# Kernel tuning notes

Hardware: AMD Instinct MI355X
Metric: run time of the kernel (lower is better)

Reference implementation:

```python
import jax, jax.numpy as jnp
import numpy as np

HEAD = 8
SR = 4
LN_EPS = 1e-5


def setup_inputs() -> dict:
    key = jax.random.key(0)
    ks = jax.random.split(key, 8)
    B, H, W, d = 4, 64, 64, 512
    s = 0.02
    inp = {
        "x": jax.random.normal(ks[0], (B, 1, H * W, d), jnp.float32),
        "Wq": jax.random.normal(ks[1], (d, d), jnp.float32) * s,
        "bq": jnp.zeros((d,), jnp.float32),
        "Wk": jax.random.normal(ks[2], (d, d), jnp.float32) * s,
        "bk": jnp.zeros((d,), jnp.float32),
        "Wv": jax.random.normal(ks[3], (d, d), jnp.float32) * s,
        "bv": jnp.zeros((d,), jnp.float32),
        "Wp": jax.random.normal(ks[4], (d, d), jnp.float32) * s,
        "bp": jnp.zeros((d,), jnp.float32),
        # spatial-reduction conv kernel, HWIO layout: [SR, SR, d, d]
        "Wsr": jax.random.normal(ks[5], (SR, SR, d, d), jnp.float32) * s,
        "bsr": jnp.zeros((d,), jnp.float32),
        "gamma": jnp.ones((d,), jnp.float32),
        "beta": jnp.zeros((d,), jnp.float32),
        "H": H,
        "W": W,
    }
    return inp


def _heads(t, B, N, dh):
    # [B, N, C] -> [B, HEAD, N, dh] ; channels split as (head, dh)
    return t.reshape(B, N, HEAD, dh).transpose(0, 2, 1, 3)


def reference(x, Wq, bq, Wk, bk, Wv, bv, Wp, bp, Wsr, bsr, gamma, beta, H, W):
    B = x.shape[0]
    C = x.shape[-1]
    dh = C // HEAD
    scale = dh ** (-0.5)
    N = H * W

    x_img = x.reshape(B, H, W, C)  # channels-last (equiv. to torch b c h w)

    # q projection (Q.Linear over channel dim)
    q = _heads((x_img @ Wq.T + bq).reshape(B, N, C), B, N, dh)  # [B,head,N,dh]

    # spatial reduction: strided conv (kernel=stride=SR) + LayerNorm over channels
    x_sr = jax.lax.conv_general_dilated(
        x_img, Wsr, window_strides=(SR, SR), padding="VALID",
        dimension_numbers=("NHWC", "HWIO", "NHWC")) + bsr  # [B,H/SR,W/SR,C]
    mu = x_sr.mean(axis=-1, keepdims=True)
    var = ((x_sr - mu) ** 2).mean(axis=-1, keepdims=True)
    x_kv = (x_sr - mu) * jax.lax.rsqrt(var + LN_EPS) * gamma + beta

    Nk = x_kv.shape[1] * x_kv.shape[2]
    x_kv = x_kv.reshape(B, Nk, C)
    k = _heads(x_kv @ Wk.T + bk, B, Nk, dh)  # [B,head,Nk,dh]
    v = _heads(x_kv @ Wv.T + bv, B, Nk, dh)  # [B,head,Nk,dh]

    attn = jnp.einsum("bhqd,bhkd->bhqk", q, k) * scale
    attn = jax.nn.softmax(attn, axis=-1)
    out = jnp.einsum("bhqk,bhkd->bhqd", attn, v)  # [B,head,N,dh]

    out = out.transpose(0, 2, 1, 3).reshape(B, N, C)
    out = out @ Wp.T + bp
    return out.reshape(B, 1, N, C)
```

## Files before the change

### kernel.cpp

```cpp
#include <hip/hip_runtime.h>


typedef __bf16 bf16x8 __attribute__((ext_vector_type(8)));
typedef float f32x4 __attribute__((ext_vector_type(4)));

__device__ __forceinline__ ushort f2bf(float v) {
  uint u = __float_as_uint(v);
  return (ushort)((u + 0x7FFFu + ((u >> 16) & 1u)) >> 16);
}
__device__ __forceinline__ float bf2f(ushort h) {
  return __uint_as_float((uint)h << 16);
}
__device__ __forceinline__ void gload16(const void* g, void* l) {
  __builtin_amdgcn_global_load_lds(
      (const __attribute__((address_space(1))) void*)g,
      (__attribute__((address_space(3))) void*)l, 16, 0, 0);
}
__device__ __forceinline__ int xcd_swz(int bid, int nwg) {
  int cpx = nwg >> 3;
  return (bid & 7) * cpx + (bid >> 3);
}

__global__ __launch_bounds__(256) void prep_kernel(
    const float* __restrict__ x, const float* __restrict__ Wq,
    const float* __restrict__ Wp, const float* __restrict__ Wk,
    const float* __restrict__ Wv, const float* __restrict__ Wsr,
    const float* __restrict__ bk, const float* __restrict__ bv,
    ushort* __restrict__ xq, ushort* __restrict__ Wq_,
    ushort* __restrict__ Wp_, ushort* __restrict__ Wkv_,
    ushort* __restrict__ Wsr_, float* __restrict__ bkv) {
  __shared__ float t[32][33];
  int bid = blockIdx.x, tid = threadIdx.x;
  if (bid < 4096 + 512) {
    const float* src;
    ushort* dst;
    int gid;
    bool full = false;
    if (bid < 4096) {
      src = x; dst = xq; gid = bid * 256 + tid;
    } else {
      int z = (bid - 4096) >> 7;
      src = (z == 0) ? Wq : (z == 1) ? Wp : (z == 2) ? Wk : Wv;
      dst = (z == 0) ? Wq_ : (z == 1) ? Wp_ : (z == 2) ? Wkv_ : (Wkv_ + 512 * 1024);
      gid = ((bid - 4096) & 127) * 256 + tid;
      full = (z >= 2);
    }
    int row = gid >> 6, c8 = (gid & 63) << 3;
    float4 a = *(const float4*)(src + (size_t)row * 512 + c8);
    float4 b = *(const float4*)(src + (size_t)row * 512 + c8 + 4);
    ushort h[8], l[8];
    float vv[8] = {a.x, a.y, a.z, a.w, b.x, b.y, b.z, b.w};
#pragma unroll
    for (int e = 0; e < 8; ++e) { h[e] = f2bf(vv[e]); l[e] = f2bf(vv[e] - bf2f(h[e])); }
    uint4 hp, lp;
    hp.x = h[0] | ((uint)h[1] << 16); hp.y = h[2] | ((uint)h[3] << 16);
    hp.z = h[4] | ((uint)h[5] << 16); hp.w = h[6] | ((uint)h[7] << 16);
    lp.x = l[0] | ((uint)l[1] << 16); lp.y = l[2] | ((uint)l[3] << 16);
    lp.z = l[4] | ((uint)l[5] << 16); lp.w = l[6] | ((uint)l[7] << 16);
    if (full) {
      *(uint4*)(dst + (size_t)row * 1024 + c8) = hp;
      *(uint4*)(dst + (size_t)row * 1024 + 512 + c8) = lp;
    } else {
      *(uint4*)(dst + (size_t)row * 512 + c8) = hp;
    }
  } else if (bid < 4096 + 512 + 4096) {
    int tb = bid - 4608;
    int z = tb >> 8, rem = tb & 255;
    int ci0 = (rem >> 4) << 5, co0 = (rem & 15) << 5;
    int tx = tid & 31, ty = tid >> 5;
#pragma unroll
    for (int i = 0; i < 32; i += 8)
      t[ty + i][tx] = Wsr[((size_t)z * 512 + ci0 + ty + i) * 512 + co0 + tx];
    __syncthreads();
#pragma unroll
    for (int i = 0; i < 32; i += 8) {
      float v = t[tx][ty + i];
      int co = co0 + ty + i, ci = ci0 + tx;
      Wsr_[((size_t)z * 512 + co) * 512 + ci] = f2bf(v);
    }
  } else {
    bkv[tid] = bk[tid]; bkv[tid + 256] = bk[tid + 256];
    bkv[tid + 512] = bv[tid]; bkv[tid + 768] = bv[tid + 256];
  }
}

template <int EPI, int TERMS>
__device__ __forceinline__ void gemm_body(
    const ushort* __restrict__ A, const ushort* __restrict__ Bw,
    const float* __restrict__ bias, float* __restrict__ C,
    ushort* __restrict__ Qs, ushort* __restrict__ Kq, ushort* __restrict__ Vt,
    int N, int bx, int by, ushort* lds) {
  constexpr int NS = (TERMS == 1) ? 8 : TERMS * 8;
  constexpr int AST = (TERMS == 1) ? 512 : 1024;
  int tid = threadIdx.x;
  int lane = tid & 63, w = tid >> 6;
  int wr = w >> 1, wc = w & 1;
  int l15 = lane & 15, g = lane >> 4;
  int srow = lane >> 3;
  int scol = (lane & 7) ^ srow;

  const ushort* aBase = A + (size_t)(by * 128 + w * 32 + srow) * AST + scol * 8;
  const ushort* bBase = Bw + (size_t)(bx * 128 + w * 32 + srow) * AST + scol * 8;

  f32x4 acc[4][4];
#pragma unroll
  for (int i = 0; i < 4; ++i)
#pragma unroll
    for (int j = 0; j < 4; ++j) acc[i][j] = (f32x4){0.f, 0.f, 0.f, 0.f};

#define STAGE_G(ks, buf)                                              \
  {                                                                   \
    int kk = (ks) * 64;                                               \
    int ap = (TERMS == 1) ? kk : kk - (kk >= 1024 ? 1024 : 0);        \
    int bp = (TERMS == 1) ? kk : kk - (kk >= 512 ? 512 : 0);          \
    ushort* aD = lds + (buf) * 16384 + w * 2048;                      \
    ushort* bD = lds + (buf) * 16384 + 8192 + w * 2048;               \
    _Pragma("unroll") for (int t = 0; t < 4; ++t) {                   \
      gload16(aBase + (size_t)t * 8 * AST + ap, aD + t * 512);        \
      gload16(bBase + (size_t)t * 8 * AST + bp, bD + t * 512);        \
    }                                                                 \
  }

#define COMPUTE_G(buf)                                                         \
  {                                                                            \
    const ushort* As = lds + (buf) * 16384;                                    \
    const ushort* Bs = As + 8192;                                              \
    _Pragma("unroll") for (int kk2 = 0; kk2 < 2; ++kk2) {                      \
      int rb = kk2 * 4 + g;                                                    \
      bf16x8 af[4], bg[4];                                                     \
      _Pragma("unroll") for (int i = 0; i < 4; ++i) {                          \
        int row = wr * 64 + i * 16 + l15;                                      \
        af[i] = *(const bf16x8*)&As[row * 64 + ((rb ^ (row & 7)) << 3)];       \
      }                                                                        \
      _Pragma("unroll") for (int j = 0; j < 4; ++j) {                          \
        int col = wc * 64 + j * 16 + l15;                                      \
        bg[j] = *(const bf16x8*)&Bs[col * 64 + ((rb ^ (col & 7)) << 3)];       \
      }                                                                        \
      _Pragma("unroll") for (int i = 0; i < 4; ++i)                            \
        _Pragma("unroll") for (int j = 0; j < 4; ++j)                          \
          acc[i][j] =                                                          \
              __builtin_amdgcn_mfma_f32_16x16x32_bf16(af[i], bg[j], acc[i][j], \
                                                      0, 0, 0);                \
    }                                                                          \
  }

  STAGE_G(0, 0);
  __syncthreads();
  for (int ks = 0; ks < NS - 1; ++ks) {
    STAGE_G(ks + 1, (ks + 1) & 1);
    COMPUTE_G(ks & 1);
    __syncthreads();
  }
  COMPUTE_G((NS - 1) & 1);

#undef STAGE_G
#undef COMPUTE_G

  if (EPI == 0) {
#pragma unroll
    for (int j = 0; j < 4; ++j) {
      int col = bx * 128 + wc * 64 + j * 16 + l15;
      float bj = bias ? bias[col] : 0.f;
#pragma unroll
      for (int i = 0; i < 4; ++i) {
        int row0 = by * 128 + wr * 64 + i * 16 + g * 4;
#pragma unroll
        for (int r = 0; r < 4; ++r)
          C[(size_t)(row0 + r) * N + col] = acc[i][j][r] + bj;
      }
    }
  } else if (EPI == 1) {
    __syncthreads();
#pragma unroll
    for (int j = 0; j < 4; ++j) {
      int cl = wc * 64 + j * 16 + l15;
      float bj = bias[bx * 128 + cl];
#pragma unroll
      for (int i = 0; i < 4; ++i) {
        int rl0 = wr * 64 + i * 16 + g * 4;
#pragma unroll
        for (int r = 0; r < 4; ++r) {
          float v = (acc[i][j][r] + bj) * 0.125f;
          ushort h = f2bf(v), lo = f2bf(v - bf2f(h));
          lds[(rl0 + r) * 128 + cl] = h;
          lds[16384 + (rl0 + r) * 128 + cl] = lo;
        }
      }
    }
    __syncthreads();
#pragma unroll
    for (int it = 0; it < 8; ++it) {
      int c = tid + it * 256;
      int r = c >> 4, ck = c & 15;
      int grow = by * 128 + r;
      size_t base = ((size_t)grow * 8 + bx * 2 + (ck >> 3)) * 128 + (ck & 7) * 8;
      *(uint4*)(Qs + base) = *(const uint4*)&lds[r * 128 + ck * 8];
      *(uint4*)(Qs + base + 64) = *(const uint4*)&lds[16384 + r * 128 + ck * 8];
    }
  } else {
#pragma unroll
    for (int j = 0; j < 4; ++j) {
      int col = bx * 128 + wc * 64 + j * 16 + l15;
      float bj = bias[col];
      bool isK = col < 512;
      int cp = isK ? col : col - 512;
      int hh = cp >> 6, d = cp & 63;
#pragma unroll
      for (int i = 0; i < 4; ++i) {
        int row0 = by * 128 + wr * 64 + i * 16 + g * 4;
#pragma unroll
        for (int r = 0; r < 4; ++r) {
          int row = row0 + r;
          int b = row >> 8, kk = row & 255;
          float v = acc[i][j][r] + bj;
          ushort h = f2bf(v), lo = f2bf(v - bf2f(h));
          if (isK) {
            size_t base = ((size_t)((b * 8 + hh) * 256) + kk) * 128 + d;
            Kq[base] = h; Kq[base + 64] = lo;
          } else {
            size_t base = ((size_t)((b * 8 + hh) * 64) + d) * 512 + kk;
            Vt[base] = h; Vt[base + 256] = lo;
          }
        }
      }
    }
  }
}

__device__ __forceinline__ void conv_body(
    const ushort* __restrict__ xq, const ushort* __restrict__ Wsr_,
    float* __restrict__ part, int bx, int by, int z, ushort* lds) {
  int kh = z >> 2, kw = z & 3;
  int tid = threadIdx.x;
  int lane = tid & 63, w = tid >> 6;
  int wr = w >> 1, wc = w & 1;
  int l15 = lane & 15, g = lane >> 4;
  int srow = lane >> 3;
  int scol = (lane & 7) ^ srow;

  const ushort* aBase[4];
#pragma unroll
  for (int t = 0; t < 4; ++t) {
    int gm = by * 128 + w * 32 + t * 8 + srow;
    int xr = (gm >> 8) * 4096 + ((((gm >> 4) & 15) << 2) + kh) * 64 +
             ((gm & 15) << 2) + kw;
    aBase[t] = xq + (size_t)xr * 512 + scol * 8;
  }
  const ushort* bBase =
      Wsr_ + ((size_t)(z * 512 + bx * 128 + w * 32 + srow)) * 512 + scol * 8;

  f32x4 acc[4][4];
#pragma unroll
  for (int i = 0; i < 4; ++i)
#pragma unroll
    for (int j = 0; j < 4; ++j) acc[i][j] = (f32x4){0.f, 0.f, 0.f, 0.f};

#define STAGE_C(ks, buf)                                              \
  {                                                                   \
    int kk = (ks) * 64;                                               \
    ushort* aD = lds + (buf) * 16384 + w * 2048;                      \
    ushort* bD = lds + (buf) * 16384 + 8192 + w * 2048;               \
    _Pragma("unroll") for (int t = 0; t < 4; ++t) {                   \
      gload16(aBase[t] + kk, aD + t * 512);                           \
      gload16(bBase + (size_t)t * 4096 + kk, bD + t * 512);           \
    }                                                                 \
  }

#define COMPUTE_C(buf)                                                         \
  {                                                                            \
    const ushort* As = lds + (buf) * 16384;                                    \
    const ushort* Bs = As + 8192;                                              \
    _Pragma("unroll") for (int kk2 = 0; kk2 < 2; ++kk2) {                      \
      int rb = kk2 * 4 + g;                                                    \
      bf16x8 af[4], bg[4];                                                     \
      _Pragma("unroll") for (int i = 0; i < 4; ++i) {                          \
        int row = wr * 64 + i * 16 + l15;                                      \
        af[i] = *(const bf16x8*)&As[row * 64 + ((rb ^ (row & 7)) << 3)];       \
      }                                                                        \
      _Pragma("unroll") for (int j = 0; j < 4; ++j) {                          \
        int col = wc * 64 + j * 16 + l15;                                      \
        bg[j] = *(const bf16x8*)&Bs[col * 64 + ((rb ^ (col & 7)) << 3)];       \
      }                                                                        \
      _Pragma("unroll") for (int i = 0; i < 4; ++i)                            \
        _Pragma("unroll") for (int j = 0; j < 4; ++j)                          \
          acc[i][j] =                                                          \
              __builtin_amdgcn_mfma_f32_16x16x32_bf16(af[i], bg[j], acc[i][j], \
                                                      0, 0, 0);                \
    }                                                                          \
  }

  STAGE_C(0, 0);
  __syncthreads();
  for (int ks = 0; ks < 7; ++ks) {
    STAGE_C(ks + 1, (ks + 1) & 1);
    COMPUTE_C(ks & 1);
    __syncthreads();
  }
  COMPUTE_C(1);

#undef STAGE_C
#undef COMPUTE_C

  float* Cp = part + (size_t)z * 524288;
#pragma unroll
  for (int j = 0; j < 4; ++j) {
    int col = bx * 128 + wc * 64 + j * 16 + l15;
#pragma unroll
    for (int i = 0; i < 4; ++i) {
      int row0 = by * 128 + wr * 64 + i * 16 + g * 4;
#pragma unroll
      for (int r = 0; r < 4; ++r)
        Cp[(size_t)(row0 + r) * 512 + col] = acc[i][j][r];
    }
  }
}

__global__ __launch_bounds__(256) void conv_kernel(
    const ushort* __restrict__ xq, const ushort* __restrict__ Wsr_,
    float* __restrict__ part) {
  __shared__ __align__(16) ushort lds[32768];
  int bid = xcd_swz(blockIdx.x, 512);
  conv_body(xq, Wsr_, part, bid & 3, (bid >> 2) & 7, bid >> 5, lds);
}

__global__ __launch_bounds__(256) void qkv_kernel(
    const ushort* __restrict__ xq, const ushort* __restrict__ Wq_,
    const float* __restrict__ bq, ushort* __restrict__ Qs,
    const ushort* __restrict__ xkv_, const ushort* __restrict__ Wkv_,
    const float* __restrict__ bkv, ushort* __restrict__ Kq,
    ushort* __restrict__ Vt) {
  __shared__ __align__(16) ushort lds[32768];
  int n = blockIdx.x;
  int xcd = n & 7, slot = n >> 3;
  if (slot < 8) {
    int id = xcd * 8 + slot;
    gemm_body<2, 3>(xkv_, Wkv_, bkv, nullptr, nullptr, Kq, Vt, 1024,
                    id & 7, id >> 3, lds);
  } else {
    int id = xcd * 64 + (slot - 8);
    gemm_body<1, 1>(xq, Wq_, bq, nullptr, Qs, nullptr, nullptr, 512,
                    id & 3, id >> 2, lds);
  }
}

__global__ __launch_bounds__(256) void gemm_out_kernel(
    const ushort* __restrict__ A, const ushort* __restrict__ Bw,
    const float* __restrict__ bias, float* __restrict__ C) {
  __shared__ __align__(16) ushort lds[32768];
  int bid = xcd_swz(blockIdx.x, 512);
  gemm_body<0, 1>(A, Bw, bias, C, nullptr, nullptr, nullptr, 512,
                  bid & 3, bid >> 2, lds);
}

__global__ __launch_bounds__(256) void ln_kernel(
    const float* __restrict__ part, const float* __restrict__ bsr,
    const float* __restrict__ gamma, const float* __restrict__ beta,
    ushort* __restrict__ xkv_) {
  int row = blockIdx.x;
  int t = threadIdx.x;
  float v0 = bsr[t], v1 = bsr[t + 256];
  for (int p = 0; p < 16; ++p) {
    v0 += part[(size_t)p * 524288 + (size_t)row * 512 + t];
    v1 += part[(size_t)p * 524288 + (size_t)row * 512 + t + 256];
  }
  float s = v0 + v1, sq = v0 * v0 + v1 * v1;
#pragma unroll
  for (int o = 1; o < 64; o <<= 1) {
    s += __shfl_xor(s, o);
    sq += __shfl_xor(sq, o);
  }
  __shared__ float red[8];
  int wv = t >> 6;
  if ((t & 63) == 0) { red[wv] = s; red[4 + wv] = sq; }
  __syncthreads();
  s = red[0] + red[1] + red[2] + red[3];
  sq = red[4] + red[5] + red[6] + red[7];
  float mu = s * (1.0f / 512.0f);
  float var = sq * (1.0f / 512.0f) - mu * mu;
  float rs = rsqrtf(var + 1e-5f);
  float y0 = (v0 - mu) * rs * gamma[t] + beta[t];
  float y1 = (v1 - mu) * rs * gamma[t + 256] + beta[t + 256];
  ushort h0 = f2bf(y0), h1 = f2bf(y1);
  xkv_[(size_t)row * 1024 + t] = h0;
  xkv_[(size_t)row * 1024 + t + 256] = h1;
  xkv_[(size_t)row * 1024 + 512 + t] = f2bf(y0 - bf2f(h0));
  xkv_[(size_t)row * 1024 + 512 + t + 256] = f2bf(y1 - bf2f(h1));
}

__global__ __launch_bounds__(256, 2) void attn_kernel(
    const ushort* __restrict__ Qs, const ushort* __restrict__ Kq,
    const ushort* __restrict__ Vt, ushort* __restrict__ attno) {
  __shared__ __align__(16) char arena[65536];
  ushort* KsL = (ushort*)arena;
  ushort* VtL = (ushort*)(arena + 16384);
  ushort* PL = (ushort*)(arena + 49152);
  float* ob = (float*)arena;

  int tid = threadIdx.x;
  int qb = blockIdx.x, h = blockIdx.y, b = blockIdx.z;
  int n0 = qb * 128, bh = b * 8 + h;
  int lane = tid & 63, w = tid >> 6;
  int q15 = lane & 15, g = lane >> 4;

  const ushort* kbase = Kq + (size_t)bh * 256 * 128;
  const ushort* vbase = Vt + (size_t)bh * 64 * 512;

  bf16x8 qf[2][2][2];
#pragma unroll
  for (int set = 0; set < 2; ++set) {
    const ushort* qptr =
        Qs + ((size_t)(b * 4096 + n0 + set * 64 + w * 16 + q15) * 8 + h) * 128;
#pragma unroll
    for (int s = 0; s < 2; ++s)
#pragma unroll
      for (int kb = 0; kb < 2; ++kb)
        qf[set][s][kb] = *(const bf16x8*)(qptr + s * 64 + kb * 32 + g * 8);
  }

  f32x4 accO[2][4];
#pragma unroll
  for (int set = 0; set < 2; ++set)
#pragma unroll
    for (int t = 0; t < 4; ++t) accO[set][t] = (f32x4){0.f, 0.f, 0.f, 0.f};
  float m[2] = {-1e30f, -1e30f}, l[2] = {0.f, 0.f};

#define STAGE_A(cc, buf)                                                     \
  {                                                                          \
    _Pragma("unroll") for (int i = 0; i < 2; ++i) {                          \
      int rb_ = w * 16 + i * 8;                                              \
      int r_ = rb_ + (lane >> 3);                                            \
      int sb_ = (lane & 7) ^ (r_ & 7);                                       \
      gload16(kbase + (size_t)((cc) * 64 + r_) * 128 + (sb_ << 3),           \
              KsL + (buf) * 4096 + rb_ * 64);                                \
    }                                                                        \
    _Pragma("unroll") for (int i = 0; i < 4; ++i) {                          \
      int rb_ = w * 16 + i * 4;                                              \
      int r_ = rb_ + (lane >> 4);                                            \
      int sb_ = (lane & 15) ^ (r_ & 7);                                      \
      gload16(vbase + (size_t)r_ * 512 + ((sb_ >> 3) << 8) + (cc) * 64 +     \
                  ((sb_ & 7) << 3),                                          \
              VtL + (buf) * 8192 + rb_ * 128);                               \
    }                                                                        \
  }

  STAGE_A(0, 0);
  __syncthreads();

  for (int c = 0; c < 4; ++c) {
    int buf = c & 1;
    if (c < 3) STAGE_A(c + 1, buf ^ 1);
    const ushort* Ks = KsL + buf * 4096;
    const ushort* Vs = VtL + buf * 8192;

    f32x4 accS[2][4];
#pragma unroll
    for (int set = 0; set < 2; ++set)
#pragma unroll
      for (int t = 0; t < 4; ++t) accS[set][t] = (f32x4){0.f, 0.f, 0.f, 0.f};
#pragma unroll
    for (int kb = 0; kb < 2; ++kb) {
      bf16x8 ak[4];
#pragma unroll
      for (int t = 0; t < 4; ++t) {
        int kkr = t * 16 + q15;
        ak[t] = *(const bf16x8*)&Ks[kkr * 64 + (((kb * 4 + g) ^ (kkr & 7)) << 3)];
      }
#pragma unroll
      for (int set = 0; set < 2; ++set) {
#pragma unroll
        for (int t = 0; t < 4; ++t)
          accS[set][t] = __builtin_amdgcn_mfma_f32_16x16x32_bf16(
              ak[t], qf[set][0][kb], accS[set][t], 0, 0, 0);
#pragma unroll
        for (int t = 0; t < 4; ++t)
          accS[set][t] = __builtin_amdgcn_mfma_f32_16x16x32_bf16(
              ak[t], qf[set][1][kb], accS[set][t], 0, 0, 0);
      }
    }

#pragma unroll
    for (int set = 0; set < 2; ++set) {
      int qrowL = set * 64 + w * 16 + q15;
      float mx = -1e30f;
#pragma unroll
      for (int t = 0; t < 4; ++t)
#pragma unroll
        for (int r = 0; r < 4; ++r) mx = fmaxf(mx, accS[set][t][r]);
      mx = fmaxf(mx, __shfl_xor(mx, 16));
      mx = fmaxf(mx, __shfl_xor(mx, 32));
      float mn = fmaxf(m[set], mx);
      float fac = __expf(m[set] - mn);
      m[set] = mn;
      float sum = 0.f;
      ushort ph[4][4];
#pragma unroll
      for (int t = 0; t < 4; ++t)
#pragma unroll
        for (int r = 0; r < 4; ++r) {
          float p = __expf(accS[set][t][r] - mn);
          ushort hp = f2bf(p);
          ph[t][r] = hp;
          sum += bf2f(hp);
        }
      sum += __shfl_xor(sum, 16);
      sum += __shfl_xor(sum, 32);
      l[set] = l[set] * fac + sum;
#pragma unroll
      for (int t = 0; t < 4; ++t) {
        accO[set][t][0] *= fac; accO[set][t][1] *= fac;
        accO[set][t][2] *= fac; accO[set][t][3] *= fac;
      }
#pragma unroll
      for (int t = 0; t < 4; ++t)
#pragma unroll
        for (int rp = 0; rp < 4; rp += 2) {
          uint u = ph[t][rp] | ((uint)ph[t][rp + 1] << 16);
          int kkl = t * 16 + g * 4 + rp;
          int blk = kkl >> 3, off = kkl & 7;
          *(uint*)((char*)PL + qrowL * 128 + ((blk ^ (q15 & 7)) << 4) + off * 2) = u;
        }
    }
    __syncthreads();

    bf16x8 pf[2][2];
#pragma unroll
    for (int set = 0; set < 2; ++set) {
      int qrowL = set * 64 + w * 16 + q15;
#pragma unroll
      for (int kb = 0; kb < 2; ++kb)
        pf[set][kb] = *(const bf16x8*)((char*)PL + qrowL * 128 +
                                       (((kb * 4 + g) ^ (q15 & 7)) << 4));
    }
#pragma unroll
    for (int s = 0; s < 2; ++s)
#pragma unroll
      for (int kb = 0; kb < 2; ++kb)
#pragma unroll
        for (int t = 0; t < 4; ++t) {
          int d = t * 16 + q15;
          bf16x8 vf =
              *(const bf16x8*)&Vs[d * 128 + (((s * 8 + kb * 4 + g) ^ (d & 7)) << 3)];
          accO[0][t] = __builtin_amdgcn_mfma_f32_16x16x32_bf16(vf, pf[0][kb],
                                                               accO[0][t], 0, 0, 0);
          accO[1][t] = __builtin_amdgcn_mfma_f32_16x16x32_bf16(vf, pf[1][kb],
                                                               accO[1][t], 0, 0, 0);
        }
    __syncthreads();
  }
#undef STAGE_A

#pragma unroll
  for (int set = 0; set < 2; ++set) {
    if (set) __syncthreads();
    float inv = 1.0f / l[set];
#pragma unroll
    for (int t = 0; t < 4; ++t)
#pragma unroll
      for (int r = 0; r < 4; ++r)
        ob[(t * 16 + g * 4 + r) * 68 + w * 16 + q15] = accO[set][t][r] * inv;
    __syncthreads();
#pragma unroll
    for (int i = 0; i < 2; ++i) {
      int idx = tid + i * 256;
      int qq = idx >> 3, d8 = (idx & 7) << 3;
      ushort hh[8];
#pragma unroll
      for (int jj = 0; jj < 8; ++jj) hh[jj] = f2bf(ob[(d8 + jj) * 68 + qq]);
      uint4 hp;
      hp.x = hh[0] | ((uint)hh[1] << 16); hp.y = hh[2] | ((uint)hh[3] << 16);
      hp.z = hh[4] | ((uint)hh[5] << 16); hp.w = hh[6] | ((uint)hh[7] << 16);
      size_t rowb = (size_t)(b * 4096 + n0 + set * 64 + qq) * 512 + h * 64 + d8;
      *(uint4*)(attno + rowb) = hp;
    }
  }
}

extern "C" void kernel_launch(void* const* d_in, const int* in_sizes, int n_in,
                              void* d_out, int out_size, void* d_ws, size_t ws_size,
                              hipStream_t stream) {
  const float* x     = (const float*)d_in[0];
  const float* Wq    = (const float*)d_in[1];
  const float* bq    = (const float*)d_in[2];
  const float* Wk    = (const float*)d_in[3];
  const float* bk    = (const float*)d_in[4];
  const float* Wv    = (const float*)d_in[5];
  const float* bv    = (const float*)d_in[6];
  const float* Wp    = (const float*)d_in[7];
  const float* bp    = (const float*)d_in[8];
  const float* Wsr   = (const float*)d_in[9];
  const float* bsr   = (const float*)d_in[10];
  const float* gamma = (const float*)d_in[11];
  const float* beta  = (const float*)d_in[12];

  float* ws = (float*)d_ws;
  ushort* xq     = (ushort*)ws;
  ushort* attno_ = (ushort*)ws;
  float*  conv_part = ws + 4194304;
  ushort* Qsplit = (ushort*)(ws + 4194304);
  ushort* Wsr_ = (ushort*)(ws + 12582912);
  float*  rest = ws + 14680064;
  ushort* Wq_  = (ushort*)rest;
  ushort* Wp_  = (ushort*)(rest + 131072);
  ushort* Wkv_ = (ushort*)(rest + 262144);
  ushort* xkv_ = (ushort*)(rest + 786432);
  ushort* Kq   = (ushort*)(rest + 1310720);
  ushort* Vt   = (ushort*)(rest + 1835008);
  float*  bkv  = rest + 2359296;
  float* outp = (float*)d_out;

  prep_kernel<<<8705, 256, 0, stream>>>(x, Wq, Wp, Wk, Wv, Wsr, bk, bv,
                                        xq, Wq_, Wp_, Wkv_, Wsr_, bkv);
  conv_kernel<<<512, 256, 0, stream>>>(xq, Wsr_, conv_part);
  ln_kernel<<<1024, 256, 0, stream>>>(conv_part, bsr, gamma, beta, xkv_);
  qkv_kernel<<<576, 256, 0, stream>>>(xq, Wq_, bq, Qsplit,
                                      xkv_, Wkv_, bkv, Kq, Vt);
  attn_kernel<<<dim3(32, 8, 4), 256, 0, stream>>>(Qsplit, Kq, Vt, attno_);
  gemm_out_kernel<<<512, 256, 0, stream>>>(attno_, Wp_, bp, outp);
}
```

Before: 120.1 us.

## Drop split-bf16 hi/lo compensation from K/V/Q paths, use plain bf16

Removes the two-term bf16 (hi+lo) representation previously used for Wk/Wv, xkv, Q, K and V, so every GEMM and the attention QK^T and PV products use single bf16 operands. This halves the K-dimension work in the KV projection and in the attention matmuls, shrinks the intermediate buffers and the attention LDS arena, and reduces global traffic. In exchange it loses the extra precision the compensation provided, which may affect accuracy against the fp32 reference.

```diff
diff --git a/kernel.cpp b/kernel.cpp
--- a/kernel.cpp
+++ b/kernel.cpp
@@ -35,34 +35,25 @@
     const float* src;
     ushort* dst;
     int gid;
-    bool full = false;
     if (bid < 4096) {
       src = x; dst = xq; gid = bid * 256 + tid;
     } else {
       int z = (bid - 4096) >> 7;
       src = (z == 0) ? Wq : (z == 1) ? Wp : (z == 2) ? Wk : Wv;
-      dst = (z == 0) ? Wq_ : (z == 1) ? Wp_ : (z == 2) ? Wkv_ : (Wkv_ + 512 * 1024);
+      dst = (z == 0) ? Wq_ : (z == 1) ? Wp_ : (z == 2) ? Wkv_ : (Wkv_ + 512 * 512);
       gid = ((bid - 4096) & 127) * 256 + tid;
-      full = (z >= 2);
     }
     int row = gid >> 6, c8 = (gid & 63) << 3;
     float4 a = *(const float4*)(src + (size_t)row * 512 + c8);
     float4 b = *(const float4*)(src + (size_t)row * 512 + c8 + 4);
-    ushort h[8], l[8];
+    ushort h[8];
     float vv[8] = {a.x, a.y, a.z, a.w, b.x, b.y, b.z, b.w};
 #pragma unroll
-    for (int e = 0; e < 8; ++e) { h[e] = f2bf(vv[e]); l[e] = f2bf(vv[e] - bf2f(h[e])); }
-    uint4 hp, lp;
+    for (int e = 0; e < 8; ++e) h[e] = f2bf(vv[e]);
+    uint4 hp;
     hp.x = h[0] | ((uint)h[1] << 16); hp.y = h[2] | ((uint)h[3] << 16);
     hp.z = h[4] | ((uint)h[5] << 16); hp.w = h[6] | ((uint)h[7] << 16);
-    lp.x = l[0] | ((uint)l[1] << 16); lp.y = l[2] | ((uint)l[3] << 16);
-    lp.z = l[4] | ((uint)l[5] << 16); lp.w = l[6] | ((uint)l[7] << 16);
-    if (full) {
-      *(uint4*)(dst + (size_t)row * 1024 + c8) = hp;
-      *(uint4*)(dst + (size_t)row * 1024 + 512 + c8) = lp;
-    } else {
-      *(uint4*)(dst + (size_t)row * 512 + c8) = hp;
-    }
+    *(uint4*)(dst + (size_t)row * 512 + c8) = hp;
   } else if (bid < 4096 + 512 + 4096) {
     int tb = bid - 4608;
     int z = tb >> 8, rem = tb & 255;
@@ -84,14 +75,12 @@
   }
 }
 
-template <int EPI, int TERMS>
+template <int EPI>
 __device__ __forceinline__ void gemm_body(
     const ushort* __restrict__ A, const ushort* __restrict__ Bw,
     const float* __restrict__ bias, float* __restrict__ C,
     ushort* __restrict__ Qs, ushort* __restrict__ Kq, ushort* __restrict__ Vt,
     int N, int bx, int by, ushort* lds) {
-  constexpr int NS = (TERMS == 1) ? 8 : TERMS * 8;
-  constexpr int AST = (TERMS == 1) ? 512 : 1024;
   int tid = threadIdx.x;
   int lane = tid & 63, w = tid >> 6;
   int wr = w >> 1, wc = w & 1;
@@ -99,8 +88,8 @@
   int srow = lane >> 3;
   int scol = (lane & 7) ^ srow;
 
-  const ushort* aBase = A + (size_t)(by * 128 + w * 32 + srow) * AST + scol * 8;
-  const ushort* bBase = Bw + (size_t)(bx * 128 + w * 32 + srow) * AST + scol * 8;
+  const ushort* aBase = A + (size_t)(by * 128 + w * 32 + srow) * 512 + scol * 8;
+  const ushort* bBase = Bw + (size_t)(bx * 128 + w * 32 + srow) * 512 + scol * 8;
 
   f32x4 acc[4][4];
 #pragma unroll
@@ -111,13 +100,11 @@
 #define STAGE_G(ks, buf)                                              \
   {                                                                   \
     int kk = (ks) * 64;                                               \
-    int ap = (TERMS == 1) ? kk : kk - (kk >= 1024 ? 1024 : 0);        \
-    int bp = (TERMS == 1) ? kk : kk - (kk >= 512 ? 512 : 0);          \
     ushort* aD = lds + (buf) * 16384 + w * 2048;                      \
     ushort* bD = lds + (buf) * 16384 + 8192 + w * 2048;               \
     _Pragma("unroll") for (int t = 0; t < 4; ++t) {                   \
-      gload16(aBase + (size_t)t * 8 * AST + ap, aD + t * 512);        \
-      gload16(bBase + (size_t)t * 8 * AST + bp, bD + t * 512);        \
+      gload16(aBase + (size_t)t * 4096 + kk, aD + t * 512);           \
+      gload16(bBase + (size_t)t * 4096 + kk, bD + t * 512);           \
     }                                                                 \
   }
 
@@ -146,12 +133,12 @@
 
   STAGE_G(0, 0);
   __syncthreads();
-  for (int ks = 0; ks < NS - 1; ++ks) {
+  for (int ks = 0; ks < 7; ++ks) {
     STAGE_G(ks + 1, (ks + 1) & 1);
     COMPUTE_G(ks & 1);
     __syncthreads();
   }
-  COMPUTE_G((NS - 1) & 1);
+  COMPUTE_G(1);
 
 #undef STAGE_G
 #undef COMPUTE_G
@@ -179,12 +166,8 @@
       for (int i = 0; i < 4; ++i) {
         int rl0 = wr * 64 + i * 16 + g * 4;
 #pragma unroll
-        for (int r = 0; r < 4; ++r) {
-          float v = (acc[i][j][r] + bj) * 0.125f;
-          ushort h = f2bf(v), lo = f2bf(v - bf2f(h));
-          lds[(rl0 + r) * 128 + cl] = h;
-          lds[16384 + (rl0 + r) * 128 + cl] = lo;
-        }
+        for (int r = 0; r < 4; ++r)
+          lds[(rl0 + r) * 128 + cl] = f2bf((acc[i][j][r] + bj) * 0.125f);
       }
     }
     __syncthreads();
@@ -193,9 +176,8 @@
       int c = tid + it * 256;
       int r = c >> 4, ck = c & 15;
       int grow = by * 128 + r;
-      size_t base = ((size_t)grow * 8 + bx * 2 + (ck >> 3)) * 128 + (ck & 7) * 8;
+      size_t base = ((size_t)grow * 8 + bx * 2 + (ck >> 3)) * 64 + (ck & 7) * 8;
       *(uint4*)(Qs + base) = *(const uint4*)&lds[r * 128 + ck * 8];
-      *(uint4*)(Qs + base + 64) = *(const uint4*)&lds[16384 + r * 128 + ck * 8];
     }
   } else {
 #pragma unroll
@@ -212,15 +194,11 @@
         for (int r = 0; r < 4; ++r) {
           int row = row0 + r;
           int b = row >> 8, kk = row & 255;
-          float v = acc[i][j][r] + bj;
-          ushort h = f2bf(v), lo = f2bf(v - bf2f(h));
-          if (isK) {
-            size_t base = ((size_t)((b * 8 + hh) * 256) + kk) * 128 + d;
-            Kq[base] = h; Kq[base + 64] = lo;
-          } else {
-            size_t base = ((size_t)((b * 8 + hh) * 64) + d) * 512 + kk;
-            Vt[base] = h; Vt[base + 256] = lo;
-          }
+          ushort h = f2bf(acc[i][j][r] + bj);
+          if (isK)
+            Kq[((size_t)((b * 8 + hh) * 256) + kk) * 64 + d] = h;
+          else
+            Vt[((size_t)((b * 8 + hh) * 64) + d) * 256 + kk] = h;
         }
       }
     }
@@ -334,12 +312,12 @@
   int xcd = n & 7, slot = n >> 3;
   if (slot < 8) {
     int id = xcd * 8 + slot;
-    gemm_body<2, 3>(xkv_, Wkv_, bkv, nullptr, nullptr, Kq, Vt, 1024,
-                    id & 7, id >> 3, lds);
+    gemm_body<2>(xkv_, Wkv_, bkv, nullptr, nullptr, Kq, Vt, 1024,
+                 id & 7, id >> 3, lds);
   } else {
     int id = xcd * 64 + (slot - 8);
-    gemm_body<1, 1>(xq, Wq_, bq, nullptr, Qs, nullptr, nullptr, 512,
-                    id & 3, id >> 2, lds);
+    gemm_body<1>(xq, Wq_, bq, nullptr, Qs, nullptr, nullptr, 512,
+                 id & 3, id >> 2, lds);
   }
 }
 
@@ -348,8 +326,8 @@
     const float* __restrict__ bias, float* __restrict__ C) {
   __shared__ __align__(16) ushort lds[32768];
   int bid = xcd_swz(blockIdx.x, 512);
-  gemm_body<0, 1>(A, Bw, bias, C, nullptr, nullptr, nullptr, 512,
-                  bid & 3, bid >> 2, lds);
+  gemm_body<0>(A, Bw, bias, C, nullptr, nullptr, nullptr, 512,
+               bid & 3, bid >> 2, lds);
 }
 
 __global__ __launch_bounds__(256) void ln_kernel(
@@ -378,22 +356,18 @@
   float mu = s * (1.0f / 512.0f);
   float var = sq * (1.0f / 512.0f) - mu * mu;
   float rs = rsqrtf(var + 1e-5f);
-  float y0 = (v0 - mu) * rs * gamma[t] + beta[t];
-  float y1 = (v1 - mu) * rs * gamma[t + 256] + beta[t + 256];
-  ushort h0 = f2bf(y0), h1 = f2bf(y1);
-  xkv_[(size_t)row * 1024 + t] = h0;
-  xkv_[(size_t)row * 1024 + t + 256] = h1;
-  xkv_[(size_t)row * 1024 + 512 + t] = f2bf(y0 - bf2f(h0));
-  xkv_[(size_t)row * 1024 + 512 + t + 256] = f2bf(y1 - bf2f(h1));
+  xkv_[(size_t)row * 512 + t] = f2bf((v0 - mu) * rs * gamma[t] + beta[t]);
+  xkv_[(size_t)row * 512 + t + 256] =
+      f2bf((v1 - mu) * rs * gamma[t + 256] + beta[t + 256]);
 }
 
 __global__ __launch_bounds__(256, 2) void attn_kernel(
     const ushort* __restrict__ Qs, const ushort* __restrict__ Kq,
     const ushort* __restrict__ Vt, ushort* __restrict__ attno) {
-  __shared__ __align__(16) char arena[65536];
+  __shared__ __align__(16) char arena[49152];
   ushort* KsL = (ushort*)arena;
   ushort* VtL = (ushort*)(arena + 16384);
-  ushort* PL = (ushort*)(arena + 49152);
+  ushort* PL = (ushort*)(arena + 32768);
   float* ob = (float*)arena;
 
   int tid = threadIdx.x;
@@ -402,19 +376,17 @@
   int lane = tid & 63, w = tid >> 6;
   int q15 = lane & 15, g = lane >> 4;
 
-  const ushort* kbase = Kq + (size_t)bh * 256 * 128;
-  const ushort* vbase = Vt + (size_t)bh * 64 * 512;
-
-  bf16x8 qf[2][2][2];
+  const ushort* kbase = Kq + (size_t)bh * 256 * 64;
+  const ushort* vbase = Vt + (size_t)bh * 64 * 256;
+
+  bf16x8 qf[2][2];
 #pragma unroll
   for (int set = 0; set < 2; ++set) {
     const ushort* qptr =
-        Qs + ((size_t)(b * 4096 + n0 + set * 64 + w * 16 + q15) * 8 + h) * 128;
-#pragma unroll
-    for (int s = 0; s < 2; ++s)
-#pragma unroll
-      for (int kb = 0; kb < 2; ++kb)
-        qf[set][s][kb] = *(const bf16x8*)(qptr + s * 64 + kb * 32 + g * 8);
+        Qs + ((size_t)(b * 4096 + n0 + set * 64 + w * 16 + q15) * 8 + h) * 64;
+#pragma unroll
+    for (int kb = 0; kb < 2; ++kb)
+      qf[set][kb] = *(const bf16x8*)(qptr + kb * 32 + g * 8);
   }
 
   f32x4 accO[2][4];
@@ -430,16 +402,10 @@
       int rb_ = w * 16 + i * 8;                                              \
       int r_ = rb_ + (lane >> 3);                                            \
       int sb_ = (lane & 7) ^ (r_ & 7);                                       \
-      gload16(kbase + (size_t)((cc) * 64 + r_) * 128 + (sb_ << 3),           \
+      gload16(kbase + (size_t)((cc) * 64 + r_) * 64 + (sb_ << 3),            \
               KsL + (buf) * 4096 + rb_ * 64);                                \
-    }                                                                        \
-    _Pragma("unroll") for (int i = 0; i < 4; ++i) {                          \
-      int rb_ = w * 16 + i * 4;                                              \
-      int r_ = rb_ + (lane >> 4);                                            \
-      int sb_ = (lane & 15) ^ (r_ & 7);                                      \
-      gload16(vbase + (size_t)r_ * 512 + ((sb_ >> 3) << 8) + (cc) * 64 +     \
-                  ((sb_ & 7) << 3),                                          \
-              VtL + (buf) * 8192 + rb_ * 128);                               \
+      gload16(vbase + (size_t)r_ * 256 + (cc) * 64 + (sb_ << 3),             \
+              VtL + (buf) * 4096 + rb_ * 64);                                \
     }                                                                        \
   }
 
@@ -450,7 +416,7 @@
     int buf = c & 1;
     if (c < 3) STAGE_A(c + 1, buf ^ 1);
     const ushort* Ks = KsL + buf * 4096;
-    const ushort* Vs = VtL + buf * 8192;
+    const ushort* Vs = VtL + buf * 4096;
 
     f32x4 accS[2][4];
 #pragma unroll
@@ -466,16 +432,11 @@
         ak[t] = *(const bf16x8*)&Ks[kkr * 64 + (((kb * 4 + g) ^ (kkr & 7)) << 3)];
       }
 #pragma unroll
-      for (int set = 0; set < 2; ++set) {
+      for (int set = 0; set < 2; ++set)
 #pragma unroll
         for (int t = 0; t < 4; ++t)
           accS[set][t] = __builtin_amdgcn_mfma_f32_16x16x32_bf16(
-              ak[t], qf[set][0][kb], accS[set][t], 0, 0, 0);
-#pragma unroll
-        for (int t = 0; t < 4; ++t)
-          accS[set][t] = __builtin_amdgcn_mfma_f32_16x16x32_bf16(
-              ak[t], qf[set][1][kb], accS[set][t], 0, 0, 0);
-      }
+              ak[t], qf[set][kb], accS[set][t], 0, 0, 0);
     }
 
 #pragma unroll
@@ -532,19 +493,17 @@
                                        (((kb * 4 + g) ^ (q15 & 7)) << 4));
     }
 #pragma unroll
-    for (int s = 0; s < 2; ++s)
-#pragma unroll
-      for (int kb = 0; kb < 2; ++kb)
-#pragma unroll
-        for (int t = 0; t < 4; ++t) {
-          int d = t * 16 + q15;
-          bf16x8 vf =
-              *(const bf16x8*)&Vs[d * 128 + (((s * 8 + kb * 4 + g) ^ (d & 7)) << 3)];
-          accO[0][t] = __builtin_amdgcn_mfma_f32_16x16x32_bf16(vf, pf[0][kb],
-                                                               accO[0][t], 0, 0, 0);
-          accO[1][t] = __builtin_amdgcn_mfma_f32_16x16x32_bf16(vf, pf[1][kb],
-                                                               accO[1][t], 0, 0, 0);
-        }
+    for (int kb = 0; kb < 2; ++kb)
+#pragma unroll
+      for (int t = 0; t < 4; ++t) {
+        int d = t * 16 + q15;
+        bf16x8 vf =
+            *(const bf16x8*)&Vs[d * 64 + (((kb * 4 + g) ^ (d & 7)) << 3)];
+        accO[0][t] = __builtin_amdgcn_mfma_f32_16x16x32_bf16(vf, pf[0][kb],
+                                                             accO[0][t], 0, 0, 0);
+        accO[1][t] = __builtin_amdgcn_mfma_f32_16x16x32_bf16(vf, pf[1][kb],
+                                                             accO[1][t], 0, 0, 0);
+      }
     __syncthreads();
   }
 #undef STAGE_A
@@ -602,10 +561,10 @@
   ushort* Wq_  = (ushort*)rest;
   ushort* Wp_  = (ushort*)(rest + 131072);
   ushort* Wkv_ = (ushort*)(rest + 262144);
-  ushort* xkv_ = (ushort*)(rest + 786432);
-  ushort* Kq   = (ushort*)(rest + 1310720);
-  ushort* Vt   = (ushort*)(rest + 1835008);
-  float*  bkv  = rest + 2359296;
+  ushort* xkv_ = (ushort*)(rest + 524288);
+  ushort* Kq   = (ushort*)(rest + 786432);
+  ushort* Vt   = (ushort*)(rest + 1048576);
+  float*  bkv  = rest + 1310720;
   float* outp = (float*)d_out;
 
   prep_kernel<<<8705, 256, 0, stream>>>(x, Wq, Wp, Wk, Wv, Wsr, bk, bv,
```

After: 99.63 us. 17.0% less time.
